# Kernel tuning notes

Hardware: AMD Instinct MI355X
Metric: run time of the kernel (lower is better)

The kernel has to match this reference:

```python
import jax, jax.numpy as jnp
import numpy as np

# Phi-3-small blocksparse config
S = 2048            # num prompt tokens (single sequence)
H = 32              # num query heads
HKV = 8             # num kv heads (GQA)
D = 128             # head size
BLK = 64            # sparse_block_size
LOCAL = 16          # local_blocks
VERT = 8            # vert_stride
SCALE = 0.08838834764831845  # 1/sqrt(128)
HEAD_SLIDE = max(1, VERT // H)  # = 1 (per-head vertical offset, homo_head=False)


def _blocksparse_mask():
    """Per-head local+strided block-sparse causal mask, shape [H, S, S] bool."""
    nb = S // BLK
    qb = jnp.arange(nb)[None, :, None]   # query block idx
    kb = jnp.arange(nb)[None, None, :]   # key block idx
    h = jnp.arange(H)[:, None, None]
    blk = (qb >= kb) & (
        (qb - kb < LOCAL) | (((kb + h * HEAD_SLIDE + 1) % VERT) == 0)
    )  # [H, nb, nb]
    dense = jnp.repeat(jnp.repeat(blk, BLK, axis=1), BLK, axis=2)  # [H, S, S]
    causal = jnp.arange(S)[:, None] >= jnp.arange(S)[None, :]
    return dense & causal[None]


def setup_inputs() -> dict:
    key = jax.random.key(0)
    k1, k2, k3 = jax.random.split(key, 3)
    return {
        "query": jax.random.normal(k1, (S, H * D), dtype=jnp.float32),
        "key": jax.random.normal(k2, (S, HKV * D), dtype=jnp.float32),
        "value": jax.random.normal(k3, (S, HKV * D), dtype=jnp.float32),
    }


def reference(query, key, value):
    q = query.reshape(S, H, D)
    k = jnp.repeat(key.reshape(S, HKV, D), H // HKV, axis=1)    # GQA expand
    v = jnp.repeat(value.reshape(S, HKV, D), H // HKV, axis=1)
    scores = jnp.einsum("qhd,khd->hqk", q, k) * SCALE           # [H, S, S]
    mask = _blocksparse_mask()
    scores = jnp.where(mask, scores, jnp.finfo(scores.dtype).min)
    p = jax.nn.softmax(scores, axis=-1)
    out = jnp.einsum("hqk,khd->qhd", p, v)                      # [S, H, D]
    return out.reshape(S, H * D)
```

## Files before the change

kernel.cpp:

```cpp
#include <hip/hip_runtime.h>


typedef __bf16 bf16_t;
typedef __bf16 bf16x4 __attribute__((ext_vector_type(4)));
typedef __bf16 bf16x8 __attribute__((ext_vector_type(8)));
typedef float  fx4    __attribute__((ext_vector_type(4)));

#define SL2E_F 0.1275240614354876f

__launch_bounds__(128, 2)
__global__ void bsfa_kernel(const float* __restrict__ Q,
                            const float* __restrict__ K,
                            const float* __restrict__ V,
                            float* __restrict__ O)
{
    const int x    = blockIdx.x;
    const int qb   = 31 - (x >> 5);
    const int h    = x & 31;
    const int kvh  = h >> 2;
    const int tid  = threadIdx.x;
    const int wv   = tid >> 6;
    const int lane = tid & 63;
    const int l15  = lane & 15;
    const int quad = lane >> 4;

    __shared__ bf16_t KsPt[64 * 136];
    __shared__ bf16_t Vt[128 * 72];

    bf16_t* Pt = &KsPt[wv * (32 * 72)];

    const int row0 = qb * 64 + wv * 32;

    bf16x8 qf[2][4];
#pragma unroll
    for (int qt = 0; qt < 2; ++qt) {
        const float* qp = Q + (size_t)(row0 + qt * 16 + l15) * 4096 + h * 128;
#pragma unroll
        for (int kc = 0; kc < 4; ++kc) {
            fx4 a = *(const fx4*)(qp + kc * 32 + quad * 8);
            fx4 b = *(const fx4*)(qp + kc * 32 + quad * 8 + 4);
            bf16x8 f;
            f[0] = (bf16_t)a[0]; f[1] = (bf16_t)a[1];
            f[2] = (bf16_t)a[2]; f[3] = (bf16_t)a[3];
            f[4] = (bf16_t)b[0]; f[5] = (bf16_t)b[1];
            f[6] = (bf16_t)b[2]; f[7] = (bf16_t)b[3];
            qf[qt][kc] = f;
        }
    }

    fx4 oacc[8][2];
    const fx4 zero4 = {0.0f, 0.0f, 0.0f, 0.0f};
#pragma unroll
    for (int dt = 0; dt < 8; ++dt)
#pragma unroll
        for (int qt = 0; qt < 2; ++qt)
            oacc[dt][qt] = zero4;

    float m_st[2] = { -1e30f, -1e30f };
    float l_st[2] = { 0.0f, 0.0f };

    const int colk = tid & 31;
    const int rowk = tid >> 5;

    for (int kb = 0; kb <= qb; ++kb) {
        if (!((qb - kb < 16) || (((kb + h + 1) & 7) == 0))) continue;

        {
            const float* kp = K + (size_t)(kb * 64) * 1024 + kvh * 128;
#pragma unroll
            for (int p = 0; p < 16; ++p) {
                const int row = p * 4 + rowk;
                fx4 xx = *(const fx4*)(kp + (size_t)row * 1024 + colk * 4);
                bf16x4 f = { (bf16_t)xx[0], (bf16_t)xx[1], (bf16_t)xx[2], (bf16_t)xx[3] };
                *(bf16x4*)&KsPt[row * 136 + colk * 4] = f;
            }
            const float* vp = V + (size_t)(kb * 64) * 1024 + kvh * 128 + tid;
#pragma unroll
            for (int kk = 0; kk < 16; ++kk) {
                const int k0 = kk * 4;
                float v0 = vp[(size_t)(k0 + 0) * 1024];
                float v1 = vp[(size_t)(k0 + 1) * 1024];
                float v2 = vp[(size_t)(k0 + 2) * 1024];
                float v3 = vp[(size_t)(k0 + 3) * 1024];
                bf16x4 f = { (bf16_t)v0, (bf16_t)v1, (bf16_t)v2, (bf16_t)v3 };
                *(bf16x4*)&Vt[tid * 72 + k0] = f;
            }
        }
        __syncthreads();

        fx4 sacc[4][2];
#pragma unroll
        for (int kt = 0; kt < 4; ++kt)
#pragma unroll
            for (int qt = 0; qt < 2; ++qt)
                sacc[kt][qt] = zero4;

#pragma unroll
        for (int kc = 0; kc < 4; ++kc)
#pragma unroll
            for (int kt = 0; kt < 4; ++kt) {
                bf16x8 kf = *(const bf16x8*)&KsPt[(kt * 16 + l15) * 136 + kc * 32 + quad * 8];
#pragma unroll
                for (int qt = 0; qt < 2; ++qt)
                    sacc[kt][qt] = __builtin_amdgcn_mfma_f32_16x16x32_bf16(
                        kf, qf[qt][kc], sacc[kt][qt], 0, 0, 0);
            }

        const bool diag = (kb == qb);
        const int qrow_in0 = wv * 32 + l15;
#pragma unroll
        for (int kt = 0; kt < 4; ++kt)
#pragma unroll
            for (int qt = 0; qt < 2; ++qt)
#pragma unroll
                for (int r = 0; r < 4; ++r) {
                    float t = sacc[kt][qt][r] * SL2E_F;
                    const int k_in = kt * 16 + quad * 4 + r;
                    const int q_in = qrow_in0 + qt * 16;
                    if (diag && (q_in < k_in)) t = -1e30f;
                    sacc[kt][qt][r] = t;
                }

#pragma unroll
        for (int qt = 0; qt < 2; ++qt) {
            float mx = sacc[0][qt][0];
#pragma unroll
            for (int kt = 0; kt < 4; ++kt)
#pragma unroll
                for (int r = 0; r < 4; ++r)
                    mx = fmaxf(mx, sacc[kt][qt][r]);
            mx = fmaxf(mx, __shfl_xor(mx, 16));
            mx = fmaxf(mx, __shfl_xor(mx, 32));
            const float mn    = fmaxf(m_st[qt], mx);
            const float alpha = exp2f(m_st[qt] - mn);
            m_st[qt] = mn;
            float rs = 0.0f;
#pragma unroll
            for (int kt = 0; kt < 4; ++kt)
#pragma unroll
                for (int r = 0; r < 4; ++r) {
                    const float p = exp2f(sacc[kt][qt][r] - mn);
                    sacc[kt][qt][r] = p;
                    rs += p;
                }
            rs += __shfl_xor(rs, 16);
            rs += __shfl_xor(rs, 32);
            l_st[qt] = l_st[qt] * alpha + rs;
#pragma unroll
            for (int dt = 0; dt < 8; ++dt)
                oacc[dt][qt] = oacc[dt][qt] * alpha;
        }

        __syncthreads();

#pragma unroll
        for (int qt = 0; qt < 2; ++qt)
#pragma unroll
            for (int kt = 0; kt < 4; ++kt) {
                bf16x4 f = { (bf16_t)sacc[kt][qt][0], (bf16_t)sacc[kt][qt][1],
                             (bf16_t)sacc[kt][qt][2], (bf16_t)sacc[kt][qt][3] };
                *(bf16x4*)&Pt[(qt * 16 + l15) * 72 + kt * 16 + quad * 4] = f;
            }
        __asm__ __volatile__("s_waitcnt lgkmcnt(0)" ::: "memory");

        bf16x8 pf[2][2];
#pragma unroll
        for (int qt = 0; qt < 2; ++qt)
#pragma unroll
            for (int kc = 0; kc < 2; ++kc)
                pf[qt][kc] = *(const bf16x8*)&Pt[(qt * 16 + l15) * 72 + kc * 32 + quad * 8];

#pragma unroll
        for (int kc = 0; kc < 2; ++kc)
#pragma unroll
            for (int dt = 0; dt < 8; ++dt) {
                bf16x8 vf = *(const bf16x8*)&Vt[(dt * 16 + l15) * 72 + kc * 32 + quad * 8];
#pragma unroll
                for (int qt = 0; qt < 2; ++qt)
                    oacc[dt][qt] = __builtin_amdgcn_mfma_f32_16x16x32_bf16(
                        vf, pf[qt][kc], oacc[dt][qt], 0, 0, 0);
            }

        __syncthreads();
    }

    const float inv0 = 1.0f / l_st[0];
    const float inv1 = 1.0f / l_st[1];
#pragma unroll
    for (int dt = 0; dt < 8; ++dt)
#pragma unroll
        for (int qt = 0; qt < 2; ++qt) {
            const float inv = qt ? inv1 : inv0;
            fx4 o = oacc[dt][qt] * inv;
            *(fx4*)(O + (size_t)(row0 + qt * 16 + l15) * 4096 + h * 128 + dt * 16 + quad * 4) = o;
        }
}

extern "C" void kernel_launch(void* const* d_in, const int* in_sizes, int n_in,
                              void* d_out, int out_size, void* d_ws, size_t ws_size,
                              hipStream_t stream) {
    (void)in_sizes; (void)n_in; (void)d_ws; (void)ws_size; (void)out_size;
    const float* q = (const float*)d_in[0];
    const float* k = (const float*)d_in[1];
    const float* v = (const float*)d_in[2];
    float* o = (float*)d_out;
    bsfa_kernel<<<dim3(1024), dim3(128), 0, stream>>>(q, k, v, o);
}
```

Baseline: 165.1 us.

## Preconvert K/V to bf16 workspace and split key blocks across waves

```diff
diff --git a/kernel.cpp b/kernel.cpp
--- a/kernel.cpp
+++ b/kernel.cpp
@@ -8,14 +8,51 @@
 
 #define SL2E_F 0.1275240614354876f
 
-__launch_bounds__(128, 2)
+__global__ void cvt_k_kernel(const float* __restrict__ K, bf16_t* __restrict__ Kb)
+{
+    const size_t i = ((size_t)blockIdx.x * 256 + threadIdx.x) * 8;
+    fx4 a = *(const fx4*)(K + i);
+    fx4 b = *(const fx4*)(K + i + 4);
+    bf16x8 f;
+    f[0] = (bf16_t)a[0]; f[1] = (bf16_t)a[1]; f[2] = (bf16_t)a[2]; f[3] = (bf16_t)a[3];
+    f[4] = (bf16_t)b[0]; f[5] = (bf16_t)b[1]; f[6] = (bf16_t)b[2]; f[7] = (bf16_t)b[3];
+    *(bf16x8*)(Kb + i) = f;
+}
+
+__global__ void transpose_v_kernel(const float* __restrict__ V, bf16_t* __restrict__ VT)
+{
+    __shared__ __align__(16) bf16_t T[64 * 72];
+    const int s0 = blockIdx.x * 64;
+    const int c0 = blockIdx.y * 64;
+    const int tx = threadIdx.x & 15, ty = threadIdx.x >> 4;
+
+    fx4 a0 = *(const fx4*)(V + (size_t)(s0 + ty * 4 + 0) * 1024 + c0 + tx * 4);
+    fx4 a1 = *(const fx4*)(V + (size_t)(s0 + ty * 4 + 1) * 1024 + c0 + tx * 4);
+    fx4 a2 = *(const fx4*)(V + (size_t)(s0 + ty * 4 + 2) * 1024 + c0 + tx * 4);
+    fx4 a3 = *(const fx4*)(V + (size_t)(s0 + ty * 4 + 3) * 1024 + c0 + tx * 4);
+#pragma unroll
+    for (int j = 0; j < 4; ++j) {
+        bf16x4 f = { (bf16_t)a0[j], (bf16_t)a1[j], (bf16_t)a2[j], (bf16_t)a3[j] };
+        *(bf16x4*)&T[(tx * 4 + j) * 72 + ty * 4] = f;
+    }
+    __syncthreads();
+    const int c = threadIdx.x >> 2, part = threadIdx.x & 3;
+    bf16x8 x0 = *(const bf16x8*)&T[c * 72 + part * 16];
+    bf16x8 x1 = *(const bf16x8*)&T[c * 72 + part * 16 + 8];
+    bf16_t* dst = VT + (size_t)(c0 + c) * 2048 + s0 + part * 16;
+    *(bf16x8*)(dst)     = x0;
+    *(bf16x8*)(dst + 8) = x1;
+}
+
+__launch_bounds__(128, 3)
 __global__ void bsfa_kernel(const float* __restrict__ Q,
-                            const float* __restrict__ K,
-                            const float* __restrict__ V,
+                            const bf16_t* __restrict__ Kb,
+                            const bf16_t* __restrict__ VT,
                             float* __restrict__ O)
 {
     const int x    = blockIdx.x;
-    const int qb   = 31 - (x >> 5);
+    const int qb   = 31 - (x >> 6);
+    const int rh   = (x >> 5) & 1;
     const int h    = x & 31;
     const int kvh  = h >> 2;
     const int tid  = threadIdx.x;
@@ -24,12 +61,11 @@
     const int l15  = lane & 15;
     const int quad = lane >> 4;
 
-    __shared__ bf16_t KsPt[64 * 136];
-    __shared__ bf16_t Vt[128 * 72];
-
-    bf16_t* Pt = &KsPt[wv * (32 * 72)];
-
-    const int row0 = qb * 64 + wv * 32;
+    __shared__ __align__(16) bf16_t Pt[2][32 * 72];
+    __shared__ float ml1m[2][16], ml1l[2][16];
+    float* Of = (float*)&Pt[0][0];
+
+    const int row0 = qb * 64 + rh * 32;
 
     bf16x8 qf[2][4];
 #pragma unroll
@@ -40,10 +76,10 @@
             fx4 a = *(const fx4*)(qp + kc * 32 + quad * 8);
             fx4 b = *(const fx4*)(qp + kc * 32 + quad * 8 + 4);
             bf16x8 f;
-            f[0] = (bf16_t)a[0]; f[1] = (bf16_t)a[1];
-            f[2] = (bf16_t)a[2]; f[3] = (bf16_t)a[3];
-            f[4] = (bf16_t)b[0]; f[5] = (bf16_t)b[1];
-            f[6] = (bf16_t)b[2]; f[7] = (bf16_t)b[3];
+            f[0] = (bf16_t)(a[0] * SL2E_F); f[1] = (bf16_t)(a[1] * SL2E_F);
+            f[2] = (bf16_t)(a[2] * SL2E_F); f[3] = (bf16_t)(a[3] * SL2E_F);
+            f[4] = (bf16_t)(b[0] * SL2E_F); f[5] = (bf16_t)(b[1] * SL2E_F);
+            f[6] = (bf16_t)(b[2] * SL2E_F); f[7] = (bf16_t)(b[3] * SL2E_F);
             qf[qt][kc] = f;
         }
     }
@@ -59,34 +95,18 @@
     float m_st[2] = { -1e30f, -1e30f };
     float l_st[2] = { 0.0f, 0.0f };
 
-    const int colk = tid & 31;
-    const int rowk = tid >> 5;
-
+    int idx = 0;
     for (int kb = 0; kb <= qb; ++kb) {
         if (!((qb - kb < 16) || (((kb + h + 1) & 7) == 0))) continue;
-
-        {
-            const float* kp = K + (size_t)(kb * 64) * 1024 + kvh * 128;
-#pragma unroll
-            for (int p = 0; p < 16; ++p) {
-                const int row = p * 4 + rowk;
-                fx4 xx = *(const fx4*)(kp + (size_t)row * 1024 + colk * 4);
-                bf16x4 f = { (bf16_t)xx[0], (bf16_t)xx[1], (bf16_t)xx[2], (bf16_t)xx[3] };
-                *(bf16x4*)&KsPt[row * 136 + colk * 4] = f;
-            }
-            const float* vp = V + (size_t)(kb * 64) * 1024 + kvh * 128 + tid;
-#pragma unroll
-            for (int kk = 0; kk < 16; ++kk) {
-                const int k0 = kk * 4;
-                float v0 = vp[(size_t)(k0 + 0) * 1024];
-                float v1 = vp[(size_t)(k0 + 1) * 1024];
-                float v2 = vp[(size_t)(k0 + 2) * 1024];
-                float v3 = vp[(size_t)(k0 + 3) * 1024];
-                bf16x4 f = { (bf16_t)v0, (bf16_t)v1, (bf16_t)v2, (bf16_t)v3 };
-                *(bf16x4*)&Vt[tid * 72 + k0] = f;
-            }
-        }
-        __syncthreads();
+        if ((idx++ & 1) != wv) continue;
+
+        const bf16_t* kbase = Kb + ((size_t)kb << 16) + (size_t)kvh * 128;
+        const bf16_t* vbase = VT + ((size_t)kvh << 18) + ((size_t)kb << 6);
+
+        bf16x8 kf[2][4];
+#pragma unroll
+        for (int kt = 0; kt < 4; ++kt)
+            kf[0][kt] = *(const bf16x8*)(kbase + (kt * 16 + l15) * 1024 + quad * 8);
 
         fx4 sacc[4][2];
 #pragma unroll
@@ -96,30 +116,33 @@
                 sacc[kt][qt] = zero4;
 
 #pragma unroll
-        for (int kc = 0; kc < 4; ++kc)
-#pragma unroll
-            for (int kt = 0; kt < 4; ++kt) {
-                bf16x8 kf = *(const bf16x8*)&KsPt[(kt * 16 + l15) * 136 + kc * 32 + quad * 8];
+        for (int kc = 0; kc < 4; ++kc) {
+            const int cur = kc & 1;
+            if (kc < 3) {
+#pragma unroll
+                for (int kt = 0; kt < 4; ++kt)
+                    kf[cur ^ 1][kt] = *(const bf16x8*)(kbase + (kt * 16 + l15) * 1024 + (kc + 1) * 32 + quad * 8);
+            }
+#pragma unroll
+            for (int kt = 0; kt < 4; ++kt)
 #pragma unroll
                 for (int qt = 0; qt < 2; ++qt)
                     sacc[kt][qt] = __builtin_amdgcn_mfma_f32_16x16x32_bf16(
-                        kf, qf[qt][kc], sacc[kt][qt], 0, 0, 0);
-            }
-
-        const bool diag = (kb == qb);
-        const int qrow_in0 = wv * 32 + l15;
-#pragma unroll
-        for (int kt = 0; kt < 4; ++kt)
-#pragma unroll
-            for (int qt = 0; qt < 2; ++qt)
-#pragma unroll
-                for (int r = 0; r < 4; ++r) {
-                    float t = sacc[kt][qt][r] * SL2E_F;
-                    const int k_in = kt * 16 + quad * 4 + r;
-                    const int q_in = qrow_in0 + qt * 16;
-                    if (diag && (q_in < k_in)) t = -1e30f;
-                    sacc[kt][qt][r] = t;
-                }
+                        kf[cur][kt], qf[qt][kc], sacc[kt][qt], 0, 0, 0);
+        }
+
+        if (kb == qb) {
+#pragma unroll
+            for (int kt = 0; kt < 4; ++kt)
+#pragma unroll
+                for (int qt = 0; qt < 2; ++qt)
+#pragma unroll
+                    for (int r = 0; r < 4; ++r) {
+                        const int k_in = kt * 16 + quad * 4 + r;
+                        const int q_in = rh * 32 + qt * 16 + l15;
+                        if (q_in < k_in) sacc[kt][qt][r] = -1e30f;
+                    }
+        }
 
 #pragma unroll
         for (int qt = 0; qt < 2; ++qt) {
@@ -151,15 +174,13 @@
                 oacc[dt][qt] = oacc[dt][qt] * alpha;
         }
 
-        __syncthreads();
-
 #pragma unroll
         for (int qt = 0; qt < 2; ++qt)
 #pragma unroll
             for (int kt = 0; kt < 4; ++kt) {
                 bf16x4 f = { (bf16_t)sacc[kt][qt][0], (bf16_t)sacc[kt][qt][1],
                              (bf16_t)sacc[kt][qt][2], (bf16_t)sacc[kt][qt][3] };
-                *(bf16x4*)&Pt[(qt * 16 + l15) * 72 + kt * 16 + quad * 4] = f;
+                *(bf16x4*)&Pt[wv][(qt * 16 + l15) * 72 + kt * 16 + quad * 4] = f;
             }
         __asm__ __volatile__("s_waitcnt lgkmcnt(0)" ::: "memory");
 
@@ -167,42 +188,78 @@
 #pragma unroll
         for (int qt = 0; qt < 2; ++qt)
 #pragma unroll
-            for (int kc = 0; kc < 2; ++kc)
-                pf[qt][kc] = *(const bf16x8*)&Pt[(qt * 16 + l15) * 72 + kc * 32 + quad * 8];
-
-#pragma unroll
-        for (int kc = 0; kc < 2; ++kc)
-#pragma unroll
-            for (int dt = 0; dt < 8; ++dt) {
-                bf16x8 vf = *(const bf16x8*)&Vt[(dt * 16 + l15) * 72 + kc * 32 + quad * 8];
+            for (int kcg = 0; kcg < 2; ++kcg)
+                pf[qt][kcg] = *(const bf16x8*)&Pt[wv][(qt * 16 + l15) * 72 + kcg * 32 + quad * 8];
+
+#pragma unroll
+        for (int kcg = 0; kcg < 2; ++kcg) {
+            bf16x8 vf[8];
+#pragma unroll
+            for (int dt = 0; dt < 8; ++dt)
+                vf[dt] = *(const bf16x8*)(vbase + (dt * 16 + l15) * 2048 + kcg * 32 + quad * 8);
+#pragma unroll
+            for (int dt = 0; dt < 8; ++dt)
 #pragma unroll
                 for (int qt = 0; qt < 2; ++qt)
                     oacc[dt][qt] = __builtin_amdgcn_mfma_f32_16x16x32_bf16(
-                        vf, pf[qt][kc], oacc[dt][qt], 0, 0, 0);
-            }
-
+                        vf[dt], pf[qt][kcg], oacc[dt][qt], 0, 0, 0);
+        }
+    }
+
+    __syncthreads();
+    if (wv == 1 && lane < 16) {
+        ml1m[0][lane] = m_st[0]; ml1m[1][lane] = m_st[1];
+        ml1l[0][lane] = l_st[0]; ml1l[1][lane] = l_st[1];
+    }
+    for (int qt = 0; qt < 2; ++qt) {
         __syncthreads();
-    }
-
-    const float inv0 = 1.0f / l_st[0];
-    const float inv1 = 1.0f / l_st[1];
-#pragma unroll
-    for (int dt = 0; dt < 8; ++dt)
-#pragma unroll
-        for (int qt = 0; qt < 2; ++qt) {
-            const float inv = qt ? inv1 : inv0;
-            fx4 o = oacc[dt][qt] * inv;
-            *(fx4*)(O + (size_t)(row0 + qt * 16 + l15) * 4096 + h * 128 + dt * 16 + quad * 4) = o;
-        }
+        if (wv == 1) {
+#pragma unroll
+            for (int dt = 0; dt < 8; ++dt)
+                *(fx4*)&Of[l15 * 132 + dt * 16 + quad * 4] = oacc[dt][qt];
+        }
+        __syncthreads();
+        if (wv == 0) {
+            const float m1 = ml1m[qt][l15], l1 = ml1l[qt][l15];
+            const float mn = fmaxf(m_st[qt], m1);
+            const float a0 = exp2f(m_st[qt] - mn);
+            const float a1 = exp2f(m1 - mn);
+            l_st[qt] = l_st[qt] * a0 + l1 * a1;
+#pragma unroll
+            for (int dt = 0; dt < 8; ++dt) {
+                fx4 of = *(const fx4*)&Of[l15 * 132 + dt * 16 + quad * 4];
+                oacc[dt][qt] = oacc[dt][qt] * a0 + of * a1;
+            }
+        }
+    }
+
+    if (wv == 0) {
+        const float inv0 = 1.0f / l_st[0];
+        const float inv1 = 1.0f / l_st[1];
+#pragma unroll
+        for (int dt = 0; dt < 8; ++dt)
+#pragma unroll
+            for (int qt = 0; qt < 2; ++qt) {
+                const float inv = qt ? inv1 : inv0;
+                fx4 o = oacc[dt][qt] * inv;
+                *(fx4*)(O + (size_t)(row0 + qt * 16 + l15) * 4096 + h * 128 + dt * 16 + quad * 4) = o;
+            }
+    }
 }
 
 extern "C" void kernel_launch(void* const* d_in, const int* in_sizes, int n_in,
                               void* d_out, int out_size, void* d_ws, size_t ws_size,
                               hipStream_t stream) {
-    (void)in_sizes; (void)n_in; (void)d_ws; (void)ws_size; (void)out_size;
+    (void)in_sizes; (void)n_in; (void)ws_size; (void)out_size;
     const float* q = (const float*)d_in[0];
     const float* k = (const float*)d_in[1];
     const float* v = (const float*)d_in[2];
     float* o = (float*)d_out;
-    bsfa_kernel<<<dim3(1024), dim3(128), 0, stream>>>(q, k, v, o);
-}
+
+    bf16_t* Kb = (bf16_t*)d_ws;
+    bf16_t* VT = Kb + (size_t)2048 * 1024;
+
+    cvt_k_kernel<<<dim3(1024), dim3(256), 0, stream>>>(k, Kb);
+    transpose_v_kernel<<<dim3(32, 16), dim3(256), 0, stream>>>(v, VT);
+    bsfa_kernel<<<dim3(2048), dim3(128), 0, stream>>>(q, Kb, VT, o);
+}
```

Measured after the change: 230.1 us. +39.4%, slower.
